# Performance work log

Hardware: AMD Instinct MI355X
Metric: run time of the kernel (lower is better)

## Reference

```python
import jax, jax.numpy as jnp
import numpy as np

B, N1, N2 = 8, 2048, 2048
K1D, K2D, V1D, V2D, AD = 256, 256, 256, 256, 128


def setup_inputs() -> dict:
    key = jax.random.key(0)
    ks = jax.random.split(key, 8)
    scale1 = 1.0 / np.sqrt(K1D)
    scale2 = 1.0 / np.sqrt(K2D)
    return {
        "k1": jax.random.normal(ks[0], (B, N1, K1D), jnp.float32),
        "k2": jax.random.normal(ks[1], (B, N2, K2D), jnp.float32),
        "v1": jax.random.normal(ks[2], (B, N1, V1D), jnp.float32),
        "v2": jax.random.normal(ks[3], (B, N2, V2D), jnp.float32),
        "W1": jax.random.uniform(ks[4], (K1D, AD), jnp.float32, -scale1, scale1),
        "b1": jax.random.uniform(ks[5], (AD,), jnp.float32, -scale1, scale1),
        "W2": jax.random.uniform(ks[6], (K2D, AD), jnp.float32, -scale2, scale2),
        "b2": jax.random.uniform(ks[7], (AD,), jnp.float32, -scale2, scale2),
    }


def reference(k1, k2, v1, v2, W1, b1, W2, b2):
    k1p = k1 @ W1 + b1                      # [B, N1, A]
    k2p = k2 @ W2 + b2                      # [B, N2, A]
    score = jnp.einsum("bnd,bmd->bnm", k1p, k2p)   # [B, N1, N2]
    w1 = jax.nn.softmax(score, axis=1)      # softmax over N1 == softmax(score^T, -1)^T
    w2 = jax.nn.softmax(score, axis=-1)     # [B, N1, N2]
    o1 = jnp.einsum("bnm,bnd->bmd", w1, v1)  # [B, N2, V1D]
    o2 = jnp.einsum("bnm,bmd->bnd", w2, v2)  # [B, N1, V2D]
    return (o2, o1)
```

## Files before the change

kernel.cpp:

```cpp
#include <hip/hip_runtime.h>
#include <hip/hip_bf16.h>

#define B_  8
#define N_  2048
#define KD_ 256
#define AD_ 128
#define VD_ 256
#define SQL2E 1.2011224087864498f

using s16x8 = __attribute__((ext_vector_type(8))) short;
using f16x8 = __attribute__((ext_vector_type(8))) _Float16;
using h2    = __attribute__((ext_vector_type(2))) __fp16;
using f32x4 = __attribute__((ext_vector_type(4))) float;

__device__ __forceinline__ f32x4 mfma16(s16x8 a, s16x8 b, f32x4 c) {
  return __builtin_amdgcn_mfma_f32_16x16x32_f16(
      __builtin_bit_cast(f16x8, a), __builtin_bit_cast(f16x8, b), c, 0, 0, 0);
}
__device__ __forceinline__ short f2h(float f) {
  _Float16 h = (_Float16)f;
  return *reinterpret_cast<short*>(&h);
}
__device__ __forceinline__ float exp2_hw(float x) {
#if __has_builtin(__builtin_amdgcn_exp2f)
  return __builtin_amdgcn_exp2f(x);
#else
  float r;
  asm volatile("v_exp_f32 %0, %1" : "=v"(r) : "v"(x));
  return r;
#endif
}
__device__ __forceinline__ s16x8 cvt8(const float* __restrict__ p) {
  union { s16x8 v; h2 h[4]; } u;
  f32x4 a = *(const f32x4*)p;
  f32x4 bq = *(const f32x4*)(p + 4);
  u.h[0] = __builtin_amdgcn_cvt_pkrtz(a[0], a[1]);
  u.h[1] = __builtin_amdgcn_cvt_pkrtz(a[2], a[3]);
  u.h[2] = __builtin_amdgcn_cvt_pkrtz(bq[0], bq[1]);
  u.h[3] = __builtin_amdgcn_cvt_pkrtz(bq[2], bq[3]);
  return u.v;
}

__global__ __launch_bounds__(256) void prep_k(
    const float* __restrict__ k1, const float* __restrict__ k2,
    const float* __restrict__ v1, const float* __restrict__ v2,
    const float* __restrict__ W1, const float* __restrict__ b1f,
    const float* __restrict__ W2, const float* __restrict__ b2f,
    short* __restrict__ q1p, short* __restrict__ q2p,
    short* __restrict__ vt1, short* __restrict__ vt2) {
  __shared__ __align__(16) short sWT[128 * 264];
  const int t  = threadIdx.x;
  const int id = blockIdx.x;

  if (id < 512) {
    const int kt = id & 31, b = (id >> 5) & 7, z = id >> 8;
    const float* src = z ? v2 : v1;
    short*       dst = z ? vt2 : vt1;
    const size_t base = ((size_t)(b * 32 + kt)) * (256 * 64);
    const int w = t >> 6, vchunk = (t >> 4) & 3, l16 = t & 15;
    #pragma unroll
    for (int i = 0; i < 8; i++) {
      float x[8];
      #pragma unroll
      for (int kk = 0; kk < 8; kk++)
        x[kk] = src[((size_t)(b * N_ + kt * 64 + i * 8 + kk)) * VD_ + t];
      union { s16x8 v; h2 h[4]; } u;
      #pragma unroll
      for (int kk = 0; kk < 4; kk++)
        u.h[kk] = __builtin_amdgcn_cvt_pkrtz(x[2 * kk], x[2 * kk + 1]);
      int f = vchunk * 2 + (i >> 2);
      *(s16x8*)&dst[base + (size_t)((w * 8 + f) * 64 + (i & 3) * 16 + l16) * 8] = u.v;
    }
    return;
  }

  const int pid = id - 512;
  const int z = pid >> 8, mb = pid & 255;
  const float* X    = z ? k2 : k1;
  const float* W    = z ? W2 : W1;
  const float* bias = z ? b2f : b1f;
  short*       Y    = z ? q2p : q1p;
  const int m0   = mb * 64;
  const int lane = t & 63, wave = t >> 6, quad = lane >> 4, l16 = lane & 15;

  #pragma unroll
  for (int j = 0; j < 64; j++) {
    int idx = j * 256 + t;
    int n = idx & 127, kh = idx >> 7;
    h2 p = __builtin_amdgcn_cvt_pkrtz(W[(size_t)(2 * kh) * AD_ + n] * SQL2E,
                                      W[(size_t)(2 * kh + 1) * AD_ + n] * SQL2E);
    *(h2*)&sWT[n * 264 + kh * 2] = p;
  }
  const float* xrow = &X[(size_t)(m0 + wave * 16 + l16) * KD_];
  s16x8 a[8];
  #pragma unroll
  for (int ks = 0; ks < 8; ks++) a[ks] = cvt8(xrow + ks * 32 + quad * 8);
  __syncthreads();

  f32x4 acc[8];
  #pragma unroll
  for (int nt = 0; nt < 8; nt++) acc[nt] = (f32x4){0.f, 0.f, 0.f, 0.f};
  #pragma unroll
  for (int ks = 0; ks < 8; ks++) {
    #pragma unroll
    for (int nt = 0; nt < 8; nt++) {
      s16x8 bf = *(const s16x8*)&sWT[(nt * 16 + l16) * 264 + ks * 32 + quad * 8];
      acc[nt] = mfma16(a[ks], bf, acc[nt]);
    }
  }
  #pragma unroll
  for (int nt = 0; nt < 8; nt++) {
    float bv = bias[nt * 16 + l16] * SQL2E;
    #pragma unroll
    for (int r = 0; r < 4; r++) {
      int row = m0 + wave * 16 + quad * 4 + r;
      Y[(size_t)row * AD_ + nt * 16 + l16] = f2h(acc[nt][r] + bv);
    }
  }
}

__global__ __launch_bounds__(256, 2) void attn_k(
    const short* __restrict__ q1p, const short* __restrict__ q2p,
    const short* __restrict__ vt1, const short* __restrict__ vt2,
    float* __restrict__ out) {
  __shared__ __align__(16) short sP[2][64 * 64];
  __shared__ __align__(16) float sMt[2][4][16][4];
  __shared__ __align__(16) float sAl[2][64];
  __shared__ __align__(16) float sL[64];

  const int t    = threadIdx.x;
  const int lane = t & 63, wave = t >> 6, quad = lane >> 4, l16 = lane & 15;
  const int id   = blockIdx.x;
  const int xcd  = id & 7, seq = id >> 3;
  const int bp   = xcd * 2 + (seq >> 5);
  const int qb   = seq & 31;
  const int b    = bp & 7, pass = bp >> 3;
  const int q0   = qb * 64;
  const short* Q  = pass ? q2p : q1p;
  const short* K  = pass ? q1p : q2p;
  const short* Vt = pass ? vt1 : vt2;
  float* O = out + (size_t)pass * ((size_t)B_ * N_ * VD_);

  const short* kp = K + ((size_t)(b * N_) + wave * 16 + l16) * AD_ + quad * 8;
  const short* vp = Vt + (size_t)b * 32 * (256 * 64) + wave * 4096 + lane * 8;

  s16x8 qf[4][4];
  #pragma unroll
  for (int qt = 0; qt < 4; qt++)
    #pragma unroll
    for (int ks = 0; ks < 4; ks++)
      qf[qt][ks] = *(const s16x8*)&Q[((size_t)(b * N_ + q0 + qt * 16 + l16)) * AD_ +
                                     ks * 32 + quad * 8];

  f32x4 m4 = (f32x4){-1e30f, -1e30f, -1e30f, -1e30f};
  f32x4 l4 = (f32x4){0.f, 0.f, 0.f, 0.f};
  f32x4 acc[16];
  #pragma unroll
  for (int c0 = 0; c0 < 16; c0++) acc[c0] = (f32x4){0.f, 0.f, 0.f, 0.f};

  s16x8 kf[4], pv[8];
  auto loadK = [&]() {
    #pragma unroll
    for (int ks = 0; ks < 4; ks++) kf[ks] = *(const s16x8*)(kp + ks * 32);
    kp += 64 * AD_;
  };
  auto loadV = [&]() {
    #pragma unroll
    for (int f = 0; f < 8; f++) pv[f] = *(const s16x8*)(vp + f * 512);
    vp += 256 * 64;
  };

  loadK();
  loadV();

  f32x4 stq[4];
  bool prevResc = false;

  for (int i = 0; i <= 32; i++) {
    const int c = i & 1;
    if (i < 32) {
      #pragma unroll
      for (int qt = 0; qt < 4; qt++) stq[qt] = (f32x4){0.f, 0.f, 0.f, 0.f};
      __builtin_amdgcn_s_setprio(1);
      #pragma unroll
      for (int ks = 0; ks < 4; ks++) {
        #pragma unroll
        for (int qt = 0; qt < 4; qt++)
          stq[qt] = mfma16(kf[ks], qf[qt][ks], stq[qt]);
      }
      __builtin_amdgcn_s_setprio(0);

      float hm0 = fmaxf(fmaxf(stq[0][0], stq[0][1]), fmaxf(stq[0][2], stq[0][3]));
      float hm1 = fmaxf(fmaxf(stq[1][0], stq[1][1]), fmaxf(stq[1][2], stq[1][3]));
      float hm2 = fmaxf(fmaxf(stq[2][0], stq[2][1]), fmaxf(stq[2][2], stq[2][3]));
      float hm3 = fmaxf(fmaxf(stq[3][0], stq[3][1]), fmaxf(stq[3][2], stq[3][3]));
      hm0 = fmaxf(hm0, __shfl_xor(hm0, 16)); hm0 = fmaxf(hm0, __shfl_xor(hm0, 32));
      hm1 = fmaxf(hm1, __shfl_xor(hm1, 16)); hm1 = fmaxf(hm1, __shfl_xor(hm1, 32));
      hm2 = fmaxf(hm2, __shfl_xor(hm2, 16)); hm2 = fmaxf(hm2, __shfl_xor(hm2, 32));
      hm3 = fmaxf(hm3, __shfl_xor(hm3, 16)); hm3 = fmaxf(hm3, __shfl_xor(hm3, 32));
      if (quad == 0) {
        f32x4 hv = (f32x4){hm0, hm1, hm2, hm3};
        *(f32x4*)&sMt[c][wave][l16][0] = hv;
      }
    }

    __syncthreads();
    if (i + 1 < 32) loadK();

    if (i > 0) {
      const int cprev = 1 - c;
      if (prevResc) {
        #pragma unroll
        for (int m = 0; m < 4; m++) {
          f32x4 aR = *(const f32x4*)&sAl[cprev][m * 16 + quad * 4];
          #pragma unroll
          for (int v = 0; v < 4; v++) {
            #pragma unroll
            for (int r = 0; r < 4; r++) acc[m * 4 + v][r] *= aR[r];
          }
        }
      }
      __builtin_amdgcn_s_setprio(1);
      #pragma unroll
      for (int m = 0; m < 4; m++) {
        #pragma unroll
        for (int ks2 = 0; ks2 < 2; ks2++) {
          int physr = (ks2 * 8 + quad * 2) ^ ((l16 & 7) << 1);
          s16x8 af = *(const s16x8*)&sP[cprev][(m * 16 + l16) * 64 + physr * 4];
          #pragma unroll
          for (int v = 0; v < 4; v++)
            acc[m * 4 + v] = mfma16(af, pv[v * 2 + ks2], acc[m * 4 + v]);
        }
      }
      __builtin_amdgcn_s_setprio(0);
      if (i < 32) loadV();
    }

    if (i < 32) {
      f32x4 w0 = *(const f32x4*)&sMt[c][0][l16][0];
      f32x4 w1 = *(const f32x4*)&sMt[c][1][l16][0];
      f32x4 w2 = *(const f32x4*)&sMt[c][2][l16][0];
      f32x4 w3 = *(const f32x4*)&sMt[c][3][l16][0];
      f32x4 mt4;
      #pragma unroll
      for (int qt = 0; qt < 4; qt++)
        mt4[qt] = fmaxf(fmaxf(w0[qt], w1[qt]), fmaxf(w2[qt], w3[qt]));

      bool ok = (mt4[0] - m4[0] <= 8.f) && (mt4[1] - m4[1] <= 8.f) &&
                (mt4[2] - m4[2] <= 8.f) && (mt4[3] - m4[3] <= 8.f);
      bool resc = !__all(ok);
      if (resc) {
        f32x4 al;
        #pragma unroll
        for (int qt = 0; qt < 4; qt++) {
          float mn = fmaxf(m4[qt], mt4[qt]);
          al[qt]  = exp2_hw(m4[qt] - mn);
          m4[qt]  = mn;
          l4[qt] *= al[qt];
        }
        if (wave == 0 && quad == 0) {
          #pragma unroll
          for (int qt = 0; qt < 4; qt++) sAl[c][qt * 16 + l16] = al[qt];
        }
      }
      prevResc = resc;

      #pragma unroll
      for (int qt = 0; qt < 4; qt++) {
        float p0 = exp2_hw(stq[qt][0] - m4[qt]);
        float p1 = exp2_hw(stq[qt][1] - m4[qt]);
        float p2 = exp2_hw(stq[qt][2] - m4[qt]);
        float p3 = exp2_hw(stq[qt][3] - m4[qt]);
        l4[qt] += (p0 + p1) + (p2 + p3);
        union { h2 h[2]; uint2 u; } wu;
        wu.h[0] = __builtin_amdgcn_cvt_pkrtz(p0, p1);
        wu.h[1] = __builtin_amdgcn_cvt_pkrtz(p2, p3);
        int phys = (wave * 4 + quad) ^ ((l16 & 7) << 1);
        *(uint2*)&sP[c][(qt * 16 + l16) * 64 + phys * 4] = wu.u;
      }
    }
  }

  #pragma unroll
  for (int qt = 0; qt < 4; qt++) {
    l4[qt] += __shfl_xor(l4[qt], 16);
    l4[qt] += __shfl_xor(l4[qt], 32);
  }
  if (quad == 0) *(f32x4*)&sMt[0][wave][l16][0] = l4;
  __syncthreads();
  if (wave == 0 && quad == 0) {
    f32x4 s0 = *(const f32x4*)&sMt[0][0][l16][0];
    f32x4 s1 = *(const f32x4*)&sMt[0][1][l16][0];
    f32x4 s2 = *(const f32x4*)&sMt[0][2][l16][0];
    f32x4 s3 = *(const f32x4*)&sMt[0][3][l16][0];
    #pragma unroll
    for (int qt = 0; qt < 4; qt++)
      sL[qt * 16 + l16] = 1.f / (s0[qt] + s1[qt] + s2[qt] + s3[qt]);
  }
  __syncthreads();
  #pragma unroll
  for (int m = 0; m < 4; m++) {
    f32x4 lv = *(const f32x4*)&sL[m * 16 + quad * 4];
    #pragma unroll
    for (int r = 0; r < 4; r++) {
      int row = q0 + m * 16 + quad * 4 + r;
      #pragma unroll
      for (int v = 0; v < 4; v++)
        O[((size_t)(b * N_ + row)) * VD_ + wave * 64 + v * 16 + l16] =
            acc[m * 4 + v][r] * lv[r];
    }
  }
}

extern "C" void kernel_launch(void* const* d_in, const int* in_sizes, int n_in,
                              void* d_out, int out_size, void* d_ws, size_t ws_size,
                              hipStream_t stream) {
  const float* k1 = (const float*)d_in[0];
  const float* k2 = (const float*)d_in[1];
  const float* v1 = (const float*)d_in[2];
  const float* v2 = (const float*)d_in[3];
  const float* W1 = (const float*)d_in[4];
  const float* b1 = (const float*)d_in[5];
  const float* W2 = (const float*)d_in[6];
  const float* b2 = (const float*)d_in[7];

  short* ws  = (short*)d_ws;
  short* q1p = ws;
  short* q2p = q1p + (size_t)16384 * 128;
  short* vt1 = q2p + (size_t)16384 * 128;
  short* vt2 = vt1 + (size_t)B_ * 32 * 256 * 64;
  float* out = (float*)d_out;

  prep_k<<<dim3(1024), dim3(256), 0, stream>>>(k1, k2, v1, v2, W1, b1, W2, b2,
                                               q1p, q2p, vt1, vt2);
  attn_k<<<dim3(512), dim3(256), 0, stream>>>(q1p, q2p, vt1, vt2, out);
}
```

Baseline: 180.6 us.

## Split attention block across eight waves with query-half and key-quarter partitioning

Doubles the attention block to 512 threads. The 8 waves split the work two ways: by query half (32 rows each) and by key quarter for the score computation, and by 32-column V slices for the PV accumulation. This halves per-wave registers (acc, qf, pv) so more waves can be resident and hide latency. The rescale decision is now shared across waves through a shared-memory flag. The cost is more shared-memory traffic and more cross-wave synchronisation in each iteration.

```diff
diff --git a/kernel.cpp b/kernel.cpp
--- a/kernel.cpp
+++ b/kernel.cpp
@@ -119,17 +119,19 @@
   }
 }
 
-__global__ __launch_bounds__(256, 2) void attn_k(
+__global__ __launch_bounds__(512, 4) void attn_k(
     const short* __restrict__ q1p, const short* __restrict__ q2p,
     const short* __restrict__ vt1, const short* __restrict__ vt2,
     float* __restrict__ out) {
   __shared__ __align__(16) short sP[2][64 * 64];
-  __shared__ __align__(16) float sMt[2][4][16][4];
+  __shared__ __align__(16) float sMt[2][2][2][4][16];
   __shared__ __align__(16) float sAl[2][64];
+  __shared__ __align__(16) float sFl[2][2];
   __shared__ __align__(16) float sL[64];
 
   const int t    = threadIdx.x;
-  const int lane = t & 63, wave = t >> 6, quad = lane >> 4, l16 = lane & 15;
+  const int lane = t & 63, w = t >> 6, quad = lane >> 4, l16 = lane & 15;
+  const int qh   = w & 1, kq = w >> 1;
   const int id   = blockIdx.x;
   const int xcd  = id & 7, seq = id >> 3;
   const int bp   = xcd * 2 + (seq >> 5);
@@ -141,24 +143,24 @@
   const short* Vt = pass ? vt1 : vt2;
   float* O = out + (size_t)pass * ((size_t)B_ * N_ * VD_);
 
-  const short* kp = K + ((size_t)(b * N_) + wave * 16 + l16) * AD_ + quad * 8;
-  const short* vp = Vt + (size_t)b * 32 * (256 * 64) + wave * 4096 + lane * 8;
-
-  s16x8 qf[4][4];
-  #pragma unroll
-  for (int qt = 0; qt < 4; qt++)
+  const short* kp = K + ((size_t)(b * N_) + kq * 16 + l16) * AD_ + quad * 8;
+  const short* vp = Vt + (size_t)b * 32 * (256 * 64) + w * 2048 + lane * 8;
+
+  s16x8 qf[2][4];
+  #pragma unroll
+  for (int qt = 0; qt < 2; qt++)
     #pragma unroll
     for (int ks = 0; ks < 4; ks++)
-      qf[qt][ks] = *(const s16x8*)&Q[((size_t)(b * N_ + q0 + qt * 16 + l16)) * AD_ +
-                                     ks * 32 + quad * 8];
-
-  f32x4 m4 = (f32x4){-1e30f, -1e30f, -1e30f, -1e30f};
-  f32x4 l4 = (f32x4){0.f, 0.f, 0.f, 0.f};
-  f32x4 acc[16];
-  #pragma unroll
-  for (int c0 = 0; c0 < 16; c0++) acc[c0] = (f32x4){0.f, 0.f, 0.f, 0.f};
-
-  s16x8 kf[4], pv[8];
+      qf[qt][ks] = *(const s16x8*)&Q[((size_t)(b * N_ + q0 + qh * 32 + qt * 16 +
+                                               l16)) * AD_ + ks * 32 + quad * 8];
+
+  float m2[2] = {-1e30f, -1e30f};
+  float l2[2] = {0.f, 0.f};
+  f32x4 acc[8];
+  #pragma unroll
+  for (int c0 = 0; c0 < 8; c0++) acc[c0] = (f32x4){0.f, 0.f, 0.f, 0.f};
+
+  s16x8 kf[4], pv[4];
   auto loadK = [&]() {
     #pragma unroll
     for (int ks = 0; ks < 4; ks++) kf[ks] = *(const s16x8*)(kp + ks * 32);
@@ -166,41 +168,35 @@
   };
   auto loadV = [&]() {
     #pragma unroll
-    for (int f = 0; f < 8; f++) pv[f] = *(const s16x8*)(vp + f * 512);
+    for (int g = 0; g < 4; g++) pv[g] = *(const s16x8*)(vp + g * 512);
     vp += 256 * 64;
   };
 
   loadK();
   loadV();
 
-  f32x4 stq[4];
-  bool prevResc = false;
+  f32x4 stq[2];
 
   for (int i = 0; i <= 32; i++) {
     const int c = i & 1;
     if (i < 32) {
-      #pragma unroll
-      for (int qt = 0; qt < 4; qt++) stq[qt] = (f32x4){0.f, 0.f, 0.f, 0.f};
+      stq[0] = (f32x4){0.f, 0.f, 0.f, 0.f};
+      stq[1] = (f32x4){0.f, 0.f, 0.f, 0.f};
       __builtin_amdgcn_s_setprio(1);
       #pragma unroll
       for (int ks = 0; ks < 4; ks++) {
-        #pragma unroll
-        for (int qt = 0; qt < 4; qt++)
-          stq[qt] = mfma16(kf[ks], qf[qt][ks], stq[qt]);
+        stq[0] = mfma16(kf[ks], qf[0][ks], stq[0]);
+        stq[1] = mfma16(kf[ks], qf[1][ks], stq[1]);
       }
       __builtin_amdgcn_s_setprio(0);
 
       float hm0 = fmaxf(fmaxf(stq[0][0], stq[0][1]), fmaxf(stq[0][2], stq[0][3]));
       float hm1 = fmaxf(fmaxf(stq[1][0], stq[1][1]), fmaxf(stq[1][2], stq[1][3]));
-      float hm2 = fmaxf(fmaxf(stq[2][0], stq[2][1]), fmaxf(stq[2][2], stq[2][3]));
-      float hm3 = fmaxf(fmaxf(stq[3][0], stq[3][1]), fmaxf(stq[3][2], stq[3][3]));
       hm0 = fmaxf(hm0, __shfl_xor(hm0, 16)); hm0 = fmaxf(hm0, __shfl_xor(hm0, 32));
       hm1 = fmaxf(hm1, __shfl_xor(hm1, 16)); hm1 = fmaxf(hm1, __shfl_xor(hm1, 32));
-      hm2 = fmaxf(hm2, __shfl_xor(hm2, 16)); hm2 = fmaxf(hm2, __shfl_xor(hm2, 32));
-      hm3 = fmaxf(hm3, __shfl_xor(hm3, 16)); hm3 = fmaxf(hm3, __shfl_xor(hm3, 32));
       if (quad == 0) {
-        f32x4 hv = (f32x4){hm0, hm1, hm2, hm3};
-        *(f32x4*)&sMt[c][wave][l16][0] = hv;
+        sMt[c][qh][0][kq][l16] = hm0;
+        sMt[c][qh][1][kq][l16] = hm1;
       }
     }
 
@@ -209,14 +205,14 @@
 
     if (i > 0) {
       const int cprev = 1 - c;
-      if (prevResc) {
+      if (sFl[cprev][0] + sFl[cprev][1] != 0.f) {
         #pragma unroll
         for (int m = 0; m < 4; m++) {
           f32x4 aR = *(const f32x4*)&sAl[cprev][m * 16 + quad * 4];
           #pragma unroll
-          for (int v = 0; v < 4; v++) {
+          for (int v = 0; v < 2; v++) {
             #pragma unroll
-            for (int r = 0; r < 4; r++) acc[m * 4 + v][r] *= aR[r];
+            for (int r = 0; r < 4; r++) acc[m * 2 + v][r] *= aR[r];
           }
         }
       }
@@ -228,8 +224,8 @@
           int physr = (ks2 * 8 + quad * 2) ^ ((l16 & 7) << 1);
           s16x8 af = *(const s16x8*)&sP[cprev][(m * 16 + l16) * 64 + physr * 4];
           #pragma unroll
-          for (int v = 0; v < 4; v++)
-            acc[m * 4 + v] = mfma16(af, pv[v * 2 + ks2], acc[m * 4 + v]);
+          for (int v = 0; v < 2; v++)
+            acc[m * 2 + v] = mfma16(af, pv[v * 2 + ks2], acc[m * 2 + v]);
         }
       }
       __builtin_amdgcn_s_setprio(0);
@@ -237,65 +233,55 @@
     }
 
     if (i < 32) {
-      f32x4 w0 = *(const f32x4*)&sMt[c][0][l16][0];
-      f32x4 w1 = *(const f32x4*)&sMt[c][1][l16][0];
-      f32x4 w2 = *(const f32x4*)&sMt[c][2][l16][0];
-      f32x4 w3 = *(const f32x4*)&sMt[c][3][l16][0];
-      f32x4 mt4;
-      #pragma unroll
-      for (int qt = 0; qt < 4; qt++)
-        mt4[qt] = fmaxf(fmaxf(w0[qt], w1[qt]), fmaxf(w2[qt], w3[qt]));
-
-      bool ok = (mt4[0] - m4[0] <= 8.f) && (mt4[1] - m4[1] <= 8.f) &&
-                (mt4[2] - m4[2] <= 8.f) && (mt4[3] - m4[3] <= 8.f);
+      float mt0 = fmaxf(fmaxf(sMt[c][qh][0][0][l16], sMt[c][qh][0][1][l16]),
+                        fmaxf(sMt[c][qh][0][2][l16], sMt[c][qh][0][3][l16]));
+      float mt1 = fmaxf(fmaxf(sMt[c][qh][1][0][l16], sMt[c][qh][1][1][l16]),
+                        fmaxf(sMt[c][qh][1][2][l16], sMt[c][qh][1][3][l16]));
+
+      bool ok   = (mt0 - m2[0] <= 8.f) && (mt1 - m2[1] <= 8.f);
       bool resc = !__all(ok);
+      float al0 = 1.f, al1 = 1.f;
       if (resc) {
-        f32x4 al;
-        #pragma unroll
-        for (int qt = 0; qt < 4; qt++) {
-          float mn = fmaxf(m4[qt], mt4[qt]);
-          al[qt]  = exp2_hw(m4[qt] - mn);
-          m4[qt]  = mn;
-          l4[qt] *= al[qt];
-        }
-        if (wave == 0 && quad == 0) {
-          #pragma unroll
-          for (int qt = 0; qt < 4; qt++) sAl[c][qt * 16 + l16] = al[qt];
-        }
-      }
-      prevResc = resc;
-
-      #pragma unroll
-      for (int qt = 0; qt < 4; qt++) {
-        float p0 = exp2_hw(stq[qt][0] - m4[qt]);
-        float p1 = exp2_hw(stq[qt][1] - m4[qt]);
-        float p2 = exp2_hw(stq[qt][2] - m4[qt]);
-        float p3 = exp2_hw(stq[qt][3] - m4[qt]);
-        l4[qt] += (p0 + p1) + (p2 + p3);
+        float mn0 = fmaxf(m2[0], mt0), mn1 = fmaxf(m2[1], mt1);
+        al0 = exp2_hw(m2[0] - mn0);  al1 = exp2_hw(m2[1] - mn1);
+        m2[0] = mn0;  m2[1] = mn1;
+        l2[0] *= al0; l2[1] *= al1;
+      }
+      if (kq == 0 && quad == 0) {
+        sAl[c][qh * 32 + l16]      = al0;
+        sAl[c][qh * 32 + 16 + l16] = al1;
+      }
+      if (kq == 0 && lane == 0) sFl[c][qh] = resc ? 1.f : 0.f;
+
+      #pragma unroll
+      for (int qt = 0; qt < 2; qt++) {
+        float mi = qt ? m2[1] : m2[0];
+        float p0 = exp2_hw(stq[qt][0] - mi);
+        float p1 = exp2_hw(stq[qt][1] - mi);
+        float p2 = exp2_hw(stq[qt][2] - mi);
+        float p3 = exp2_hw(stq[qt][3] - mi);
+        l2[qt] += (p0 + p1) + (p2 + p3);
         union { h2 h[2]; uint2 u; } wu;
         wu.h[0] = __builtin_amdgcn_cvt_pkrtz(p0, p1);
         wu.h[1] = __builtin_amdgcn_cvt_pkrtz(p2, p3);
-        int phys = (wave * 4 + quad) ^ ((l16 & 7) << 1);
-        *(uint2*)&sP[c][(qt * 16 + l16) * 64 + phys * 4] = wu.u;
-      }
-    }
-  }
-
-  #pragma unroll
-  for (int qt = 0; qt < 4; qt++) {
-    l4[qt] += __shfl_xor(l4[qt], 16);
-    l4[qt] += __shfl_xor(l4[qt], 32);
-  }
-  if (quad == 0) *(f32x4*)&sMt[0][wave][l16][0] = l4;
+        int phys = (kq * 4 + quad) ^ ((l16 & 7) << 1);
+        *(uint2*)&sP[c][(qh * 32 + qt * 16 + l16) * 64 + phys * 4] = wu.u;
+      }
+    }
+  }
+
+  l2[0] += __shfl_xor(l2[0], 16); l2[0] += __shfl_xor(l2[0], 32);
+  l2[1] += __shfl_xor(l2[1], 16); l2[1] += __shfl_xor(l2[1], 32);
+  if (quad == 0) {
+    sMt[0][qh][0][kq][l16] = l2[0];
+    sMt[0][qh][1][kq][l16] = l2[1];
+  }
   __syncthreads();
-  if (wave == 0 && quad == 0) {
-    f32x4 s0 = *(const f32x4*)&sMt[0][0][l16][0];
-    f32x4 s1 = *(const f32x4*)&sMt[0][1][l16][0];
-    f32x4 s2 = *(const f32x4*)&sMt[0][2][l16][0];
-    f32x4 s3 = *(const f32x4*)&sMt[0][3][l16][0];
-    #pragma unroll
-    for (int qt = 0; qt < 4; qt++)
-      sL[qt * 16 + l16] = 1.f / (s0[qt] + s1[qt] + s2[qt] + s3[qt]);
+  if (w < 4 && quad == 0) {
+    int eh = w & 1, et = w >> 1;
+    float s = sMt[0][eh][et][0][l16] + sMt[0][eh][et][1][l16] +
+              sMt[0][eh][et][2][l16] + sMt[0][eh][et][3][l16];
+    sL[eh * 32 + et * 16 + l16] = 1.f / s;
   }
   __syncthreads();
   #pragma unroll
@@ -305,9 +291,9 @@
     for (int r = 0; r < 4; r++) {
       int row = q0 + m * 16 + quad * 4 + r;
       #pragma unroll
-      for (int v = 0; v < 4; v++)
-        O[((size_t)(b * N_ + row)) * VD_ + wave * 64 + v * 16 + l16] =
-            acc[m * 4 + v][r] * lv[r];
+      for (int v = 0; v < 2; v++)
+        O[((size_t)(b * N_ + row)) * VD_ + w * 32 + v * 16 + l16] =
+            acc[m * 2 + v][r] * lv[r];
     }
   }
 }
@@ -333,5 +319,5 @@
 
   prep_k<<<dim3(1024), dim3(256), 0, stream>>>(k1, k2, v1, v2, W1, b1, W2, b2,
                                                q1p, q2p, vt1, vt2);
-  attn_k<<<dim3(512), dim3(256), 0, stream>>>(q1p, q2p, vt1, vt2, out);
-}
+  attn_k<<<dim3(512), dim3(512), 0, stream>>>(q1p, q2p, vt1, vt2, out);
+}
```

Result: slower. 261.8 us (+45.0%).
